# Performance work log

Hardware: AMD Instinct MI355X
Metric: run time of the kernel (lower is better)

Reference implementation:

```python
import jax, jax.numpy as jnp
import numpy as np

# Product-key memory config (matches init_kwargs)
HEADS = 4
K_DIM = 512          # per-head query/key dim; split in two halves of 256
HALF = K_DIM // 2
V_DIM = 512
SUBSIZE = 512        # sub-keys per bank; value table size = SUBSIZE**2
SIZE = SUBSIZE * SUBSIZE
TOPK = 8
TEMP = 1.0
B, T = 4, 2048


def setup_inputs() -> dict:
    key = jax.random.key(0)
    kq, kk, kv = jax.random.split(key, 3)
    bound = 1.0 / np.sqrt(K_DIM)  # reset_parameters: uniform(-1/sqrt(k_dim), 1/sqrt(k_dim))
    query = jax.random.normal(kq, (B, T, HEADS * K_DIM), dtype=jnp.float32)
    keys = jax.random.uniform(kk, (2 * HEADS * SUBSIZE, HALF), dtype=jnp.float32,
                              minval=-bound, maxval=bound)
    # reset_parameters: normal(0, v_dim**-0.5)
    values = jax.random.normal(kv, (SIZE, V_DIM), dtype=jnp.float32) * (V_DIM ** -0.5)
    return {"query": query, "keys": keys, "values": values}


def reference(query, keys, values):
    """retrieve_values: product-key two-stage topk + softmax-weighted embedding bag.
    query: [B, T, HEADS*K_DIM]; keys: [2*HEADS*SUBSIZE, HALF]; values: [SIZE, V_DIM]
    returns retrieved values [B*T, V_DIM].
    """
    Bq, Tq = query.shape[:2]
    N = Bq * Tq
    q = query.reshape(N, HEADS, K_DIM)
    q1, q2 = q[..., :HALF], q[..., HALF:]
    k = keys.reshape(2, HEADS, SUBSIZE, HALF)

    # Sub-key score matmuls (the two 'cdist-like' searches)
    s1 = jnp.einsum('nhd,hsd->nhs', q1, k[0])       # [N, H, SUBSIZE]
    s2 = jnp.einsum('nhd,hsd->nhs', q2, k[1])       # [N, H, SUBSIZE]

    ts1, ti1 = jax.lax.top_k(s1, TOPK)               # [N, H, TOPK]
    ts2, ti2 = jax.lax.top_k(s2, TOPK)

    # Cartesian combination of the two topk sets, then global topk
    comb = (ts1[..., :, None] + ts2[..., None, :]).reshape(N, HEADS, TOPK * TOPK)
    scores, flat_idx = jax.lax.top_k(comb, TOPK)     # [N, H, TOPK]
    sel1 = jnp.take_along_axis(ti1, flat_idx // TOPK, axis=-1)
    sel2 = jnp.take_along_axis(ti2, flat_idx % TOPK, axis=-1)
    indices = sel1 * SUBSIZE + sel2                  # global value-table indices [N, H, TOPK]

    # score_transform: softmax over heads*topk (score_nonlinear='softmax')
    w = jax.nn.softmax(scores.reshape(N, HEADS * TOPK) / TEMP, axis=-1)

    # xformers_embedding_bag: weighted gather-sum over the huge value table
    gathered = values[indices.reshape(N, HEADS * TOPK)]   # [N, H*TOPK, V_DIM]
    vals = jnp.einsum('nk,nkd->nd', w, gathered)          # [N, V_DIM]
    return vals
```

## Files before the change

### kernel.cpp

```cpp
#include <hip/hip_runtime.h>
#include <hip/hip_bf16.h>
#include <math.h>

typedef unsigned short u16;
typedef __attribute__((ext_vector_type(8))) short short8;
typedef __attribute__((ext_vector_type(4))) float f32x4;

#define N_TOK   8192
#define N_HEADS 4
#define KDIM    512
#define HALFD   256
#define VDIM    512
#define SUBK    512
#define NCAND   16

__device__ __forceinline__ u16 f2bf(float f) {
    unsigned u = __float_as_uint(f);
    u += 0x7fffu + ((u >> 16) & 1u);
    return (u16)(u >> 16);
}

__device__ __forceinline__ unsigned med3u(unsigned a, unsigned b, unsigned c) {
    unsigned d;
    asm("v_med3_u32 %0, %1, %2, %3" : "=v"(d) : "v"(a), "v"(b), "v"(c));
    return d;
}

__global__ void k_convert(const float* __restrict__ in, u16* __restrict__ out, int n4) {
    int i = blockIdx.x * blockDim.x + threadIdx.x;
    int stride = gridDim.x * blockDim.x;
    for (; i < n4; i += stride) {
        float4 v = ((const float4*)in)[i];
        unsigned a = (unsigned)f2bf(v.x) | ((unsigned)f2bf(v.y) << 16);
        unsigned b = (unsigned)f2bf(v.z) | ((unsigned)f2bf(v.w) << 16);
        ((uint2*)out)[i] = make_uint2(a, b);
    }
}

__global__ __launch_bounds__(256) void k_score_topk(
    const float* __restrict__ query,
    const u16* __restrict__ kb,
    int* __restrict__ cand)
{
    __shared__ unsigned sc[16 * 513];
    const int nb = blockIdx.x, h = blockIdx.y, half = blockIdx.z;
    const int tid = threadIdx.x;
    const int wave = tid >> 6, l = tid & 63;
    const int lr = l & 15, lk = l >> 4;

    const float* qbase = query + (size_t)(nb * 16 + lr) * (N_HEADS * KDIM)
                       + h * KDIM + half * HALFD + lk * 8;
    short8 a[8];
#pragma unroll
    for (int kf = 0; kf < 8; ++kf) {
        float4 q0 = *(const float4*)(qbase + kf * 32);
        float4 q1 = *(const float4*)(qbase + kf * 32 + 4);
        short8 t;
        t[0] = (short)f2bf(q0.x); t[1] = (short)f2bf(q0.y);
        t[2] = (short)f2bf(q0.z); t[3] = (short)f2bf(q0.w);
        t[4] = (short)f2bf(q1.x); t[5] = (short)f2bf(q1.y);
        t[6] = (short)f2bf(q1.z); t[7] = (short)f2bf(q1.w);
        a[kf] = t;
    }

    const u16* kbase = kb + (size_t)(half * N_HEADS + h) * SUBK * HALFD;
#pragma unroll
    for (int t = 0; t < 8; ++t) {
        const int st = wave * 8 + t;
        const u16* kp = kbase + (size_t)(st * 16 + lr) * HALFD + lk * 8;
        short8 b[8];
#pragma unroll
        for (int kf = 0; kf < 8; ++kf)
            b[kf] = *(const short8*)(kp + kf * 32);
        f32x4 acc = {0.f, 0.f, 0.f, 0.f};
#pragma unroll
        for (int kf = 0; kf < 8; ++kf)
            acc = __builtin_amdgcn_mfma_f32_16x16x32_bf16(a[kf], b[kf], acc, 0, 0, 0);
#pragma unroll
        for (int r = 0; r < 4; ++r) {
            unsigned ub = __float_as_uint(acc[r]);
            unsigned key = ub ^ ((unsigned)((int)ub >> 31) | 0x80000000u);
            key = (key & 0xFFFFFE00u) | (unsigned)(st * 16 + lr);
            sc[(lk * 4 + r) * 513 + st * 16 + lr] = key;
        }
    }
    __syncthreads();

    const int row = tid >> 4, sub = tid & 15;
    unsigned tv[NCAND];
#pragma unroll
    for (int j = 0; j < NCAND; ++j) tv[j] = 0u;
    const int base = row * 513 + sub;
#pragma unroll
    for (int t = 0; t < 32; ++t) {
        unsigned v = sc[base + (t << 4)];
#pragma unroll
        for (int j = NCAND - 1; j >= 1; --j)
            tv[j] = med3u(tv[j - 1], tv[j], v);
        tv[0] = (tv[0] > v) ? tv[0] : v;
    }

    unsigned keep = 0;
#pragma unroll
    for (int r = 0; r < NCAND; ++r) {
        unsigned w = tv[0];
#pragma unroll
        for (int d = 1; d < 16; d <<= 1) {
            unsigned o = __shfl_xor(w, d, 16);
            w = (o > w) ? o : w;
        }
        if (sub == r) keep = w;
        bool pop = (tv[0] == w);
#pragma unroll
        for (int j = 0; j < NCAND - 1; ++j) tv[j] = pop ? tv[j + 1] : tv[j];
        tv[NCAND - 1] = pop ? 0u : tv[NCAND - 1];
    }
    const int n = nb * 16 + row;
    cand[((size_t)n * 8 + (h * 2 + half)) * NCAND + sub] = (int)(keep & 0x1FFu);
}

__global__ __launch_bounds__(256) void k_select(
    const float* __restrict__ query,
    const float* __restrict__ keys,
    const int* __restrict__ cand,
    int* __restrict__ gout,
    float* __restrict__ wout)
{
    __shared__ double rv[8][16];
    __shared__ int    ri[8][16];
    __shared__ double tsv[8][8];
    __shared__ int    tsi[8][8];
    __shared__ double s_comb[32];
    __shared__ int    sgi[32];

    const int n = blockIdx.x;
    const int tid = threadIdx.x;

    {
        const int dot = tid >> 1, part = tid & 1;
        const int g = dot >> 4, j = dot & 15;
        const int h = g >> 1, half = g & 1;
        const int sidx = cand[((size_t)n * 8 + g) * NCAND + j];
        const float* qrow = query + (size_t)n * (N_HEADS * KDIM) + h * KDIM + half * HALFD + part * 128;
        const float* krow = keys + ((size_t)(half * N_HEADS + h) * SUBK + sidx) * HALFD + part * 128;
        double a0 = 0, a1 = 0, a2 = 0, a3 = 0;
#pragma unroll 8
        for (int d = 0; d < 128; d += 4) {
            float4 qv = *(const float4*)(qrow + d);
            float4 kv = *(const float4*)(krow + d);
            a0 = fma((double)qv.x, (double)kv.x, a0);
            a1 = fma((double)qv.y, (double)kv.y, a1);
            a2 = fma((double)qv.z, (double)kv.z, a2);
            a3 = fma((double)qv.w, (double)kv.w, a3);
        }
        double s = (a0 + a1) + (a2 + a3);
        double o = __shfl_xor(s, 1);
        if (part == 0) { rv[g][j] = s + o; ri[g][j] = sidx; }
    }
    __syncthreads();

    if (tid < 128) {
        const int g = tid >> 4, j = tid & 15;
        double v = rv[g][j];
        const int idx = ri[g][j];
        for (int r = 0; r < 8; ++r) {
            double bv = v; int bj = j;
#pragma unroll
            for (int d = 1; d < 16; d <<= 1) {
                double ov = __shfl_xor(bv, d, 16);
                int    oj = __shfl_xor(bj, d, 16);
                if (ov > bv || (ov == bv && oj < bj)) { bv = ov; bj = oj; }
            }
            int widx = __shfl(idx, bj, 16);
            if (j == r) { tsv[g][r] = bv; tsi[g][r] = widx; }
            if (j == bj) v = -1e300;
        }
    }
    __syncthreads();

    {
        const int h = tid >> 6, f = tid & 63;
        double c = tsv[h * 2][f >> 3] + tsv[h * 2 + 1][f & 7];
        for (int r = 0; r < 8; ++r) {
            double bv = c; int bf = f;
#pragma unroll
            for (int d = 1; d < 64; d <<= 1) {
                double ov = __shfl_xor(bv, d, 64);
                int    of = __shfl_xor(bf, d, 64);
                if (ov > bv || (ov == bv && of < bf)) { bv = ov; bf = of; }
            }
            if (f == r) {
                s_comb[h * 8 + r] = bv;
                sgi[h * 8 + r] = tsi[h * 2][bf >> 3] * SUBK + tsi[h * 2 + 1][bf & 7];
            }
            if (f == bf) c = -1e300;
        }
    }
    __syncthreads();

    if (tid < 32) {
        const int k = tid;
        double s = s_comb[k];
        double m = s;
#pragma unroll
        for (int d = 1; d < 32; d <<= 1) m = fmax(m, __shfl_xor(m, d, 32));
        float e = expf((float)(s - m));
        float sum = e;
#pragma unroll
        for (int d = 1; d < 32; d <<= 1) sum += __shfl_xor(sum, d, 32);
        wout[(size_t)n * 32 + k] = e / sum;
        gout[(size_t)n * 32 + k] = sgi[k];
    }
}

__global__ __launch_bounds__(256) void k_gather(
    const float* __restrict__ values,
    const int* __restrict__ gidx,
    const float* __restrict__ w,
    float* __restrict__ out)
{
    __shared__ float    ws_[32];
    __shared__ unsigned off2_[32];
    const int n = blockIdx.x;
    const int tid = threadIdx.x;
    if (tid < 32) {
        ws_[tid] = w[(size_t)n * 32 + tid];
        off2_[tid] = (unsigned)gidx[(size_t)n * 32 + tid] * 256u;
    }
    __syncthreads();

    const float2* v2 = (const float2*)values;
    float2 v[32];
#pragma unroll
    for (int k = 0; k < 32; ++k)
        v[k] = v2[(size_t)off2_[k] + (unsigned)tid];

    float a0 = 0.f, a1 = 0.f;
#pragma unroll
    for (int k = 0; k < 32; ++k) {
        float wk = ws_[k];
        a0 = fmaf(wk, v[k].x, a0);
        a1 = fmaf(wk, v[k].y, a1);
    }
    ((float2*)(out + (size_t)n * VDIM))[tid] = make_float2(a0, a1);
}

extern "C" void kernel_launch(void* const* d_in, const int* in_sizes, int n_in,
                              void* d_out, int out_size, void* d_ws, size_t ws_size,
                              hipStream_t stream) {
    const float* query  = (const float*)d_in[0];
    const float* keys   = (const float*)d_in[1];
    const float* values = (const float*)d_in[2];
    float* out = (float*)d_out;

    char* ws = (char*)d_ws;
    u16* kb    = (u16*)ws;
    int* cand  = (int*)(ws + 2097152);
    int* gidxb = (int*)(ws + 2097152 + 4194304);
    float* wb  = (float*)(ws + 2097152 + 4194304 + 1048576);

    k_convert<<<512, 256, 0, stream>>>(keys, kb, (2 * N_HEADS * SUBK * HALFD) / 4);

    dim3 gB(N_TOK / 16, N_HEADS, 2);
    k_score_topk<<<gB, 256, 0, stream>>>(query, kb, cand);

    k_select<<<N_TOK, 256, 0, stream>>>(query, keys, cand, gidxb, wb);
    k_gather<<<N_TOK, 256, 0, stream>>>(values, gidxb, wb, out);
}
```

Measured before the change: 409.6 us.

## Fuse select and gather kernels, split gather across four waves

Merges the selection/softmax kernel and the weighted value gather into one kernel, so the indices and weights never round-trip through global memory and one launch is removed. Within the fused kernel, each of the four wavefronts gathers 8 of the 32 value rows using float4 loads, and the partial sums are reduced through shared memory. This adds 8 KB of shared memory and two extra barriers per block, and the gather now runs after the serial select phase instead of in an independent kernel, which may reduce latency hiding. It also issues fewer loads in flight per thread (8 float4 per batch instead of 32 float2).

After: 387.8 us. 5.3% less time.

```diff
diff --git a/kernel.cpp b/kernel.cpp
--- a/kernel.cpp
+++ b/kernel.cpp
@@ -119,12 +119,12 @@
     cand[((size_t)n * 8 + (h * 2 + half)) * NCAND + sub] = (int)(keep & 0x1FFu);
 }
 
-__global__ __launch_bounds__(256) void k_select(
+__global__ __launch_bounds__(256) void k_select_gather(
     const float* __restrict__ query,
     const float* __restrict__ keys,
+    const float* __restrict__ values,
     const int* __restrict__ cand,
-    int* __restrict__ gout,
-    float* __restrict__ wout)
+    float* __restrict__ out)
 {
     __shared__ double rv[8][16];
     __shared__ int    ri[8][16];
@@ -132,17 +132,19 @@
     __shared__ int    tsi[8][8];
     __shared__ double s_comb[32];
     __shared__ int    sgi[32];
+    __shared__ float  wsm[32];
+    __shared__ float  part[4][512];
 
     const int n = blockIdx.x;
     const int tid = threadIdx.x;
 
     {
-        const int dot = tid >> 1, part = tid & 1;
+        const int dot = tid >> 1, pt = tid & 1;
         const int g = dot >> 4, j = dot & 15;
         const int h = g >> 1, half = g & 1;
         const int sidx = cand[((size_t)n * 8 + g) * NCAND + j];
-        const float* qrow = query + (size_t)n * (N_HEADS * KDIM) + h * KDIM + half * HALFD + part * 128;
-        const float* krow = keys + ((size_t)(half * N_HEADS + h) * SUBK + sidx) * HALFD + part * 128;
+        const float* qrow = query + (size_t)n * (N_HEADS * KDIM) + h * KDIM + half * HALFD + pt * 128;
+        const float* krow = keys + ((size_t)(half * N_HEADS + h) * SUBK + sidx) * HALFD + pt * 128;
         double a0 = 0, a1 = 0, a2 = 0, a3 = 0;
 #pragma unroll 8
         for (int d = 0; d < 128; d += 4) {
@@ -155,7 +157,7 @@
         }
         double s = (a0 + a1) + (a2 + a3);
         double o = __shfl_xor(s, 1);
-        if (part == 0) { rv[g][j] = s + o; ri[g][j] = sidx; }
+        if (pt == 0) { rv[g][j] = s + o; ri[g][j] = sidx; }
     }
     __syncthreads();
 
@@ -208,41 +210,48 @@
         float sum = e;
 #pragma unroll
         for (int d = 1; d < 32; d <<= 1) sum += __shfl_xor(sum, d, 32);
-        wout[(size_t)n * 32 + k] = e / sum;
-        gout[(size_t)n * 32 + k] = sgi[k];
-    }
-}
-
-__global__ __launch_bounds__(256) void k_gather(
-    const float* __restrict__ values,
-    const int* __restrict__ gidx,
-    const float* __restrict__ w,
-    float* __restrict__ out)
-{
-    __shared__ float    ws_[32];
-    __shared__ unsigned off2_[32];
-    const int n = blockIdx.x;
-    const int tid = threadIdx.x;
-    if (tid < 32) {
-        ws_[tid] = w[(size_t)n * 32 + tid];
-        off2_[tid] = (unsigned)gidx[(size_t)n * 32 + tid] * 256u;
-    }
-    __syncthreads();
-
-    const float2* v2 = (const float2*)values;
-    float2 v[32];
-#pragma unroll
-    for (int k = 0; k < 32; ++k)
-        v[k] = v2[(size_t)off2_[k] + (unsigned)tid];
-
-    float a0 = 0.f, a1 = 0.f;
-#pragma unroll
-    for (int k = 0; k < 32; ++k) {
-        float wk = ws_[k];
-        a0 = fmaf(wk, v[k].x, a0);
-        a1 = fmaf(wk, v[k].y, a1);
-    }
-    ((float2*)(out + (size_t)n * VDIM))[tid] = make_float2(a0, a1);
+        wsm[k] = e / sum;
+    }
+    __syncthreads();
+
+    {
+        const int w = tid >> 6, lane = tid & 63;
+        float4 acc0 = {0.f, 0.f, 0.f, 0.f};
+        float4 acc1 = {0.f, 0.f, 0.f, 0.f};
+#pragma unroll
+        for (int b = 0; b < 2; ++b) {
+            float4 v0[4], v1[4];
+#pragma unroll
+            for (int r = 0; r < 4; ++r) {
+                const int k = w * 8 + b * 4 + r;
+                const float* vr = values + (size_t)sgi[k] * VDIM;
+                v0[r] = *(const float4*)(vr + lane * 4);
+                v1[r] = *(const float4*)(vr + 256 + lane * 4);
+            }
+#pragma unroll
+            for (int r = 0; r < 4; ++r) {
+                const float wk = wsm[w * 8 + b * 4 + r];
+                acc0.x = fmaf(wk, v0[r].x, acc0.x);
+                acc0.y = fmaf(wk, v0[r].y, acc0.y);
+                acc0.z = fmaf(wk, v0[r].z, acc0.z);
+                acc0.w = fmaf(wk, v0[r].w, acc0.w);
+                acc1.x = fmaf(wk, v1[r].x, acc1.x);
+                acc1.y = fmaf(wk, v1[r].y, acc1.y);
+                acc1.z = fmaf(wk, v1[r].z, acc1.z);
+                acc1.w = fmaf(wk, v1[r].w, acc1.w);
+            }
+        }
+        *(float4*)(&part[w][lane * 4]) = acc0;
+        *(float4*)(&part[w][256 + lane * 4]) = acc1;
+    }
+    __syncthreads();
+
+    {
+        const int c = tid * 2;
+        float s0 = part[0][c]     + part[1][c]     + part[2][c]     + part[3][c];
+        float s1 = part[0][c + 1] + part[1][c + 1] + part[2][c + 1] + part[3][c + 1];
+        ((float2*)(out + (size_t)n * VDIM))[tid] = make_float2(s0, s1);
+    }
 }
 
 extern "C" void kernel_launch(void* const* d_in, const int* in_sizes, int n_in,
@@ -254,16 +263,13 @@
     float* out = (float*)d_out;
 
     char* ws = (char*)d_ws;
-    u16* kb    = (u16*)ws;
-    int* cand  = (int*)(ws + 2097152);
-    int* gidxb = (int*)(ws + 2097152 + 4194304);
-    float* wb  = (float*)(ws + 2097152 + 4194304 + 1048576);
+    u16* kb   = (u16*)ws;
+    int* cand = (int*)(ws + 2097152);
 
     k_convert<<<512, 256, 0, stream>>>(keys, kb, (2 * N_HEADS * SUBK * HALFD) / 4);
 
     dim3 gB(N_TOK / 16, N_HEADS, 2);
     k_score_topk<<<gB, 256, 0, stream>>>(query, kb, cand);
 
-    k_select<<<N_TOK, 256, 0, stream>>>(query, keys, cand, gidxb, wb);
-    k_gather<<<N_TOK, 256, 0, stream>>>(values, gidxb, wb, out);
-}
+    k_select_gather<<<N_TOK, 256, 0, stream>>>(query, keys, values, cand, out);
+}
```
